# Optimization experiments

Measured on AMD Instinct MI355X. Metric: run time of the kernel, lower is better.

Reference implementation:

```python
import jax, jax.numpy as jnp
import numpy as np

NF = 3
THRESH = 0.05
MODES1 = [0, 64, 32]
MODES2 = [0, 64, 32]
LEVEL = 3
WIDTHS = [32, 64, 64]


def _cgelu(z):
    # split-complex GELU: gelu on real and imag parts independently
    return jax.nn.gelu(z.real) + 1j * jax.nn.gelu(z.imag)


def _forward(x_real, x_imag, Re,
             p_w1_r, p_w1_i, p_b1_r, p_b1_i, p_w2_r, p_w2_i, p_b2_r, p_b2_i,
             w0_r, w0_i, wd1_r, wd1_i, wu1_r, wu1_i, wd2_r, wd2_i, wu2_r, wu2_i,
             S1, S2):
    c = lambda r, i: (r + 1j * i).astype(jnp.complex64)
    x = c(x_real, x_imag)                       # (B, C0, S1, M2) half-spectrum
    B = x.shape[0]
    M1, M2 = S1 // 2, S2 // 2 + 1
    m1_list = [M1, MODES1[1], MODES1[2]]
    m2_list = [M2, MODES2[1], MODES2[2]]

    # --- get_k: fractional powers of signed wavenumbers ---
    h1, h2 = S1 // 2, S2 // 2
    kx1 = jnp.concatenate([jnp.arange(0, S1 - h1), jnp.arange(-h1, 0)]).reshape(S1, 1)
    kx2 = jnp.concatenate([jnp.arange(0, S2 - h2), jnp.arange(-h2, 0)]).reshape(1, S2)
    k = jnp.stack([jnp.broadcast_to(kx1, (S1, S2)),
                   jnp.broadcast_to(kx2, (S1, S2))], 0)[..., :M2]   # (2, S1, M2)
    pw = (jnp.arange(1, NF + 1, dtype=jnp.float32) / NF).reshape(NF, 1, 1, 1)
    k_mat = jnp.power(k[None].astype(jnp.complex64), pw)            # (NF, 2, S1, M2)
    k_mat = jnp.broadcast_to(k_mat.reshape(1, 2 * NF, S1, M2), (B, 2 * NF, S1, M2))

    # --- embed_re: fractional powers of Reynolds number ---
    re_pw = (jnp.arange(1, NF + 1, dtype=jnp.float32) / NF).reshape(1, NF, 1, 1)
    re_mat = jnp.power(Re, re_pw).astype(jnp.complex64)             # (B, NF, 1, 1)
    re_mat = jnp.broadcast_to(re_mat, (B, NF, S1, M2))

    feat = jnp.concatenate([k_mat, re_mat], axis=1)                 # (B, 3*NF, S1, M2)

    # --- complex 1x1-conv MLP p ---
    h = jnp.einsum('bixy,oi->boxy', feat, c(p_w1_r, p_w1_i)) + c(p_b1_r, p_b1_i)[None, :, None, None]
    h = _cgelu(h)
    re_feature = jnp.einsum('bixy,oi->boxy', h, c(p_w2_r, p_w2_i)) + c(p_b2_r, p_b2_i)[None, :, None, None]

    x = x * re_feature
    x = jnp.where(jnp.abs(x) > THRESH, x, jnp.zeros((), x.dtype))   # sparsity mask

    # level 0 (skip_in is all-ones complex)
    x1 = x + 1.0
    x1 = _cgelu(jnp.einsum('bixy,io->boxy', x1, c(w0_r, w0_i)))

    Wd = [None, c(wd1_r, wd1_i), c(wd2_r, wd2_i)]
    Wu = [None, c(wu1_r, wu1_i), c(wu2_r, wu2_i)]

    xs = [x1]
    for i in range(1, LEVEL):  # down path: corner mode truncation + channel mix
        m1, m2 = m1_list[i], m2_list[i]
        x2 = jnp.concatenate([x1[:, :, :m1, :m2], x1[:, :, -m1:, :m2]], axis=2)
        x1 = _cgelu(jnp.einsum('bixy,io->boxy', x2, Wd[i])) + 1.0
        xs.append(x1)

    skip_out = list(xs)
    for i in range(LEVEL - 1, 0, -1):  # up path: channel mix + corner add
        u = _cgelu(jnp.einsum('bixy,io->boxy', xs[i], Wu[i]))
        m1, m2 = m1_list[i], m2_list[i]
        prev = xs[i - 1]
        prev = prev.at[:, :, :m1, :m2].add(u[:, :, :m1, :m2])
        prev = prev.at[:, :, -m1:, :m2].add(u[:, :, -m1:, :m2])
        xs[i - 1] = prev
        skip_out[i - 1] = prev  # torch mutates in place, so skip_out aliases

    return (xs[0], skip_out[0], skip_out[1], skip_out[2])


def setup_inputs() -> dict:
    key = jax.random.key(0)
    B, S1, S2 = 8, 256, 256
    M2 = S2 // 2 + 1
    ks = jax.random.split(key, 24)
    f = lambda k, s: jax.random.normal(k, s, jnp.float32)
    w = lambda k, s: 0.05 * jax.random.normal(k, s, jnp.float32)
    return {
        'x_real': f(ks[0], (B, 32, S1, M2)),
        'x_imag': f(ks[1], (B, 32, S1, M2)),
        'Re': jax.random.uniform(ks[2], (B, 1, 1, 1), jnp.float32, 0.5, 2.0),
        'p_w1_r': w(ks[3], (32, 9)), 'p_w1_i': w(ks[4], (32, 9)),
        'p_b1_r': w(ks[5], (32,)), 'p_b1_i': w(ks[6], (32,)),
        'p_w2_r': w(ks[7], (32, 32)), 'p_w2_i': w(ks[8], (32, 32)),
        'p_b2_r': w(ks[9], (32,)), 'p_b2_i': w(ks[10], (32,)),
        'w0_r': w(ks[11], (32, 32)), 'w0_i': w(ks[12], (32, 32)),
        'wd1_r': w(ks[13], (32, 64)), 'wd1_i': w(ks[14], (32, 64)),
        'wu1_r': w(ks[15], (64, 32)), 'wu1_i': w(ks[16], (64, 32)),
        'wd2_r': w(ks[17], (64, 64)), 'wd2_i': w(ks[18], (64, 64)),
        'wu2_r': w(ks[19], (64, 64)), 'wu2_i': w(ks[20], (64, 64)),
        'S1': S1, 'S2': S2,
    }


def reference(x_real, x_imag, Re,
              p_w1_r, p_w1_i, p_b1_r, p_b1_i, p_w2_r, p_w2_i, p_b2_r, p_b2_i,
              w0_r, w0_i, wd1_r, wd1_i, wu1_r, wu1_i, wd2_r, wd2_i, wu2_r, wu2_i,
              S1, S2):
    return _forward(x_real, x_imag, Re,
                    p_w1_r, p_w1_i, p_b1_r, p_b1_i, p_w2_r, p_w2_i, p_b2_r, p_b2_i,
                    w0_r, w0_i, wd1_r, wd1_i, wu1_r, wu1_i, wd2_r, wd2_i, wu2_r, wu2_i,
                    S1, S2)
```

## Files before the change

### kernel.cpp

```cpp
#include <hip/hip_runtime.h>

typedef long long i64;

#define BB   8
#define SS1  256
#define MM2  129
#define SP0  (SS1*MM2)

#define O0 0LL
#define O1 8454144LL
#define O2 16908288LL
#define O3 21102592LL

__device__ __forceinline__ float ldf(const float* p, i64 i, i64 cap) {
    return (i >= 0 && i < cap) ? p[i] : 0.0f;
}
__device__ __forceinline__ void stf(float* p, i64 i, i64 cap, float v) {
    if (i >= 0 && i < cap) p[i] = v;
}

__device__ __forceinline__ float tanh_fast(float x) {
    float a = fabsf(x);
    float t = __expf(-2.0f * a);
    float r = (1.0f - t) * __builtin_amdgcn_rcpf(1.0f + t);
    return copysignf(r, x);
}
__device__ __forceinline__ float gelu_f(float x) {
    float inner = 0.7978845608028654f * (x + 0.044715f * x * x * x);
    return 0.5f * x * (1.0f + tanh_fast(inner));
}

__device__ __forceinline__ void compute_features(
    int b, int x, int y, const float* __restrict__ Re,
    float* fr, float* fi, float* rp)
{
    float kv0 = (x < 128) ? (float)x : (float)(x - 256);
    float kv1 = (y < 128) ? (float)y : -128.0f;
    const float P[3] = {1.0f/3.0f, 2.0f/3.0f, 1.0f};
    #pragma unroll
    for (int d = 0; d < 2; d++) {
        float k = d ? kv1 : kv0;
        float lg = __logf(fabsf(k));
        #pragma unroll
        for (int f = 0; f < 3; f++) {
            int c = f * 2 + d;
            float m = __expf(P[f] * lg);
            if (k == 0.0f)      { fr[c] = 0.0f; fi[c] = 0.0f; }
            else if (k > 0.0f)  { fr[c] = m;    fi[c] = 0.0f; }
            else {
                float ang = P[f] * 3.14159274101257f;
                fr[c] = m * __cosf(ang);
                fi[c] = m * __sinf(ang);
            }
        }
    }
    float lre = __logf(Re[b]);
    #pragma unroll
    for (int f = 0; f < 3; f++) rp[f] = __expf(P[f] * lre);
}

__global__ __launch_bounds__(256) void k_level0(
    const float* __restrict__ xr, const float* __restrict__ xi,
    const float* __restrict__ Re,
    const float* __restrict__ w1r, const float* __restrict__ w1i,
    const float* __restrict__ b1r, const float* __restrict__ b1i,
    const float* __restrict__ w2r, const float* __restrict__ w2i,
    const float* __restrict__ b2r, const float* __restrict__ b2i,
    const float* __restrict__ w0r, const float* __restrict__ w0i,
    float* __restrict__ of, i64 capf)
{
    int idx = blockIdx.x * 256 + threadIdx.x;
    if (idx >= BB * SP0) return;
    int y  = idx % MM2;
    int t2 = idx / MM2;
    int x  = t2 % SS1;
    int b  = t2 / SS1;

    float fr[6], fi[6], rp[3];
    compute_features(b, x, y, Re, fr, fi, rp);

    float hr[32], hi[32];
    #pragma unroll
    for (int o = 0; o < 32; o++) {
        float ar = b1r[o], ai = b1i[o];
        #pragma unroll
        for (int i = 0; i < 6; i++) {
            float wr = w1r[o * 9 + i], wi = w1i[o * 9 + i];
            ar += wr * fr[i] - wi * fi[i];
            ai += wr * fi[i] + wi * fr[i];
        }
        #pragma unroll
        for (int f = 0; f < 3; f++) {
            ar += w1r[o * 9 + 6 + f] * rp[f];
            ai += w1i[o * 9 + 6 + f] * rp[f];
        }
        hr[o] = gelu_f(ar);
        hi[o] = gelu_f(ai);
    }

    float acc[32];
    #pragma unroll
    for (int o = 0; o < 32; o++) acc[o] = 0.0f;

    const float TH2 = 0.05f * 0.05f;
    i64 base0 = (i64)b * 32 * SP0 + (i64)x * MM2 + y;
    for (int c = 0; c < 32; c++) {
        float rr0 = b2r[c], ri0 = b2i[c], rr1 = 0.0f, ri1 = 0.0f;
        #pragma unroll
        for (int i = 0; i < 16; i++) {
            float wr = w2r[c * 32 + i], wi = w2i[c * 32 + i];
            rr0 += wr * hr[i] - wi * hi[i];
            ri0 += wr * hi[i] + wi * hr[i];
        }
        #pragma unroll
        for (int i = 16; i < 32; i++) {
            float wr = w2r[c * 32 + i], wi = w2i[c * 32 + i];
            rr1 += wr * hr[i] - wi * hi[i];
            ri1 += wr * hi[i] + wi * hr[i];
        }
        float rrs = rr0 + rr1, ris = ri0 + ri1;
        float xre = xr[base0 + (i64)c * SP0];
        float xim = xi[base0 + (i64)c * SP0];
        float pr = xre * rrs - xim * ris;
        float pi = xre * ris + xim * rrs;
        if (pr * pr + pi * pi <= TH2) { pr = 0.0f; pi = 0.0f; }
        float vr_c = pr + 1.0f;
        float vi_c = pi;
        #pragma unroll
        for (int o = 0; o < 32; o++) {
            float wr = w0r[c * 32 + o], wi = w0i[c * 32 + o];
            acc[o] += wr * vr_c - wi * vi_c;
        }
    }

    #pragma unroll
    for (int o = 0; o < 32; o++) {
        float g = gelu_f(acc[o]);
        i64 oi = base0 + (i64)o * SP0;
        stf(of, O0 + oi, capf, g);
        stf(of, O1 + oi, capf, g);
    }
}

#define PH  0
#define PV  32
#define PX1 64
#define PV1 96
#define PV2 160

__global__ __launch_bounds__(512, 4) void k_branch1(
    const float* __restrict__ xr, const float* __restrict__ xi,
    const float* __restrict__ Re,
    const float* __restrict__ w1r, const float* __restrict__ w1i,
    const float* __restrict__ b1r, const float* __restrict__ b1i,
    const float* __restrict__ w2r, const float* __restrict__ w2i,
    const float* __restrict__ b2r, const float* __restrict__ b2i,
    const float* __restrict__ w0r, const float* __restrict__ w0i,
    const float* __restrict__ wd1r, const float* __restrict__ wd1i,
    const float* __restrict__ wu1r, const float* __restrict__ wu1i,
    float* __restrict__ of, i64 capf)
{
    int base = blockIdx.x * 8;
    int y0 = base & 63;
    int r1 = (base >> 6) & 127;
    int b  = base >> 13;
    if ((y0 < 32) && (r1 < 32 || r1 >= 96)) return;
    int x0 = (r1 < 64) ? r1 : r1 + 128;

    __shared__ float2 s_w2t[1024];
    __shared__ float2 s_w0[1024];
    __shared__ float2 s_wd1[2048];
    __shared__ float2 s_wu1[2048];
    __shared__ float2 s_pt[8][160];
    __shared__ float  s_u[8][32];

    for (int t = threadIdx.x; t < 1024; t += 512) {
        int c = t >> 5, i = t & 31;
        s_w2t[i * 32 + c] = make_float2(w2r[t], w2i[t]);
        s_w0[t] = make_float2(w0r[t], w0i[t]);
    }
    for (int t = threadIdx.x; t < 2048; t += 512) {
        s_wd1[t] = make_float2(wd1r[t], wd1i[t]);
        s_wu1[t] = make_float2(wu1r[t], wu1i[t]);
    }

    int p = threadIdx.x >> 6;
    int lane = threadIdx.x & 63;
    int y = y0 + p;

    if (lane < 32) {
        float fr[6], fi[6], rp[3];
        compute_features(b, x0, y, Re, fr, fi, rp);
        int o = lane;
        float ar = b1r[o], ai = b1i[o];
        #pragma unroll
        for (int i = 0; i < 6; i++) {
            float wr = w1r[o * 9 + i], wi = w1i[o * 9 + i];
            ar += wr * fr[i] - wi * fi[i];
            ai += wr * fi[i] + wi * fr[i];
        }
        #pragma unroll
        for (int f = 0; f < 3; f++) {
            ar += w1r[o * 9 + 6 + f] * rp[f];
            ai += w1i[o * 9 + 6 + f] * rp[f];
        }
        s_pt[p][PH + o] = make_float2(gelu_f(ar), gelu_f(ai));
    }
    __syncthreads();

    if (lane < 32) {
        int c = lane;
        float rr = b2r[c], ri = b2i[c];
        #pragma unroll
        for (int i = 0; i < 32; i++) {
            float2 w = s_w2t[i * 32 + c];
            float2 h = s_pt[p][PH + i];
            rr += w.x * h.x - w.y * h.y;
            ri += w.x * h.y + w.y * h.x;
        }
        i64 xoff = ((i64)b * 32 + c) * SP0 + (i64)x0 * MM2 + y;
        float xre = xr[xoff], xim = xi[xoff];
        float pr = xre * rr - xim * ri;
        float pi = xre * ri + xim * rr;
        const float TH2 = 0.05f * 0.05f;
        if (pr * pr + pi * pi <= TH2) { pr = 0.0f; pi = 0.0f; }
        s_pt[p][PV + c] = make_float2(pr + 1.0f, pi);
    }
    __syncthreads();

    {
        int o = lane & 31, part = lane >> 5;
        const float* vv = (const float*)&s_pt[p][PV];
        int ia = part ? 1 : 0, ib = part ? 0 : 1;
        float sgn = part ? 1.0f : -1.0f;
        float a = 0.0f;
        #pragma unroll
        for (int c2 = 0; c2 < 32; c2++) {
            float2 w = s_w0[c2 * 32 + o];
            a += w.x * vv[2 * c2 + ia] + sgn * w.y * vv[2 * c2 + ib];
        }
        a = gelu_f(a);
        ((float*)&s_pt[p][PX1 + o])[part] = a;
    }
    __syncthreads();

    {
        float ar = 0.0f, ai = 0.0f;
        #pragma unroll
        for (int i2 = 0; i2 < 32; i2++) {
            float2 w = s_wd1[i2 * 64 + lane];
            float2 x1 = s_pt[p][PX1 + i2];
            ar += w.x * x1.x - w.y * x1.y;
            ai += w.x * x1.y + w.y * x1.x;
        }
        s_pt[p][PV1 + lane] = make_float2(gelu_f(ar) + 1.0f, gelu_f(ai));
    }
    __syncthreads();

    {
        int o = threadIdx.x >> 3, ty = threadIdx.x & 7;
        float v = s_pt[ty][PV1 + o].x;
        stf(of, O2 + ((i64)((i64)b * 64 + o) * 128 + r1) * 64 + (y0 + ty), capf, v);
    }

    {
        int o = lane & 31, half = lane >> 5;
        float acc = 0.0f;
        #pragma unroll
        for (int c2 = 0; c2 < 32; c2++) {
            int c = half * 32 + c2;
            float2 w = s_wu1[c * 32 + o];
            float2 v1 = s_pt[p][PV1 + c];
            acc += w.x * v1.x - w.y * v1.y;
        }
        acc += __shfl_xor(acc, 32);
        if (lane < 32) s_u[p][o] = gelu_f(acc);
    }
    __syncthreads();

    if (threadIdx.x < 256) {
        int o = threadIdx.x >> 3, ty = threadIdx.x & 7;
        i64 oi = ((i64)b * 32 + o) * SP0 + (i64)x0 * MM2 + (y0 + ty);
        float cur = ldf(of, O0 + oi, capf) + s_u[ty][o];
        stf(of, O0 + oi, capf, cur);
        stf(of, O1 + oi, capf, cur);
    }
}

__global__ __launch_bounds__(512, 4) void k_branch2(
    const float* __restrict__ xr, const float* __restrict__ xi,
    const float* __restrict__ Re,
    const float* __restrict__ w1r, const float* __restrict__ w1i,
    const float* __restrict__ b1r, const float* __restrict__ b1i,
    const float* __restrict__ w2r, const float* __restrict__ w2i,
    const float* __restrict__ b2r, const float* __restrict__ b2i,
    const float* __restrict__ w0r, const float* __restrict__ w0i,
    const float* __restrict__ wd1r, const float* __restrict__ wd1i,
    const float* __restrict__ wu1r, const float* __restrict__ wu1i,
    const float* __restrict__ wd2r, const float* __restrict__ wd2i,
    const float* __restrict__ wu2r, const float* __restrict__ wu2i,
    float* __restrict__ of, i64 capf)
{
    int base = blockIdx.x * 8;
    int y0 = base & 31;
    int r2 = (base >> 5) & 63;
    int b  = base >> 11;
    int r1 = (r2 < 32) ? r2 : r2 + 64;
    int x0 = (r1 < 64) ? r1 : r1 + 128;

    __shared__ float2 s_w2t[1024];
    __shared__ float2 s_w0[1024];
    __shared__ float2 s_wd1[2048];
    __shared__ float2 s_wu1[2048];
    __shared__ float2 s_pt[8][224];
    __shared__ float  s_u[8][32];

    for (int t = threadIdx.x; t < 1024; t += 512) {
        int c = t >> 5, i = t & 31;
        s_w2t[i * 32 + c] = make_float2(w2r[t], w2i[t]);
        s_w0[t] = make_float2(w0r[t], w0i[t]);
    }
    for (int t = threadIdx.x; t < 2048; t += 512) {
        s_wd1[t] = make_float2(wd1r[t], wd1i[t]);
        s_wu1[t] = make_float2(wu1r[t], wu1i[t]);
    }

    int p = threadIdx.x >> 6;
    int lane = threadIdx.x & 63;
    int y = y0 + p;

    if (lane < 32) {
        float fr[6], fi[6], rp[3];
        compute_features(b, x0, y, Re, fr, fi, rp);
        int o = lane;
        float ar = b1r[o], ai = b1i[o];
        #pragma unroll
        for (int i = 0; i < 6; i++) {
            float wr = w1r[o * 9 + i], wi = w1i[o * 9 + i];
            ar += wr * fr[i] - wi * fi[i];
            ai += wr * fi[i] + wi * fr[i];
        }
        #pragma unroll
        for (int f = 0; f < 3; f++) {
            ar += w1r[o * 9 + 6 + f] * rp[f];
            ai += w1i[o * 9 + 6 + f] * rp[f];
        }
        s_pt[p][PH + o] = make_float2(gelu_f(ar), gelu_f(ai));
    }
    __syncthreads();

    if (lane < 32) {
        int c = lane;
        float rr = b2r[c], ri = b2i[c];
        #pragma unroll
        for (int i = 0; i < 32; i++) {
            float2 w = s_w2t[i * 32 + c];
            float2 h = s_pt[p][PH + i];
            rr += w.x * h.x - w.y * h.y;
            ri += w.x * h.y + w.y * h.x;
        }
        i64 xoff = ((i64)b * 32 + c) * SP0 + (i64)x0 * MM2 + y;
        float xre = xr[xoff], xim = xi[xoff];
        float pr = xre * rr - xim * ri;
        float pi = xre * ri + xim * rr;
        const float TH2 = 0.05f * 0.05f;
        if (pr * pr + pi * pi <= TH2) { pr = 0.0f; pi = 0.0f; }
        s_pt[p][PV + c] = make_float2(pr + 1.0f, pi);
    }
    __syncthreads();

    {
        int o = lane & 31, part = lane >> 5;
        const float* vv = (const float*)&s_pt[p][PV];
        int ia = part ? 1 : 0, ib = part ? 0 : 1;
        float sgn = part ? 1.0f : -1.0f;
        float a = 0.0f;
        #pragma unroll
        for (int c2 = 0; c2 < 32; c2++) {
            float2 w = s_w0[c2 * 32 + o];
            a += w.x * vv[2 * c2 + ia] + sgn * w.y * vv[2 * c2 + ib];
        }
        a = gelu_f(a);
        ((float*)&s_pt[p][PX1 + o])[part] = a;
    }
    __syncthreads();

    {
        float ar = 0.0f, ai = 0.0f;
        #pragma unroll
        for (int i2 = 0; i2 < 32; i2++) {
            float2 w = s_wd1[i2 * 64 + lane];
            float2 x1 = s_pt[p][PX1 + i2];
            ar += w.x * x1.x - w.y * x1.y;
            ai += w.x * x1.y + w.y * x1.x;
        }
        s_pt[p][PV1 + lane] = make_float2(gelu_f(ar) + 1.0f, gelu_f(ai));
    }
    __syncthreads();

    {
        float ar = 0.0f, ai = 0.0f;
        #pragma unroll 8
        for (int c2 = 0; c2 < 64; c2++) {
            float wr = wd2r[c2 * 64 + lane], wi = wd2i[c2 * 64 + lane];
            float2 v1 = s_pt[p][PV1 + c2];
            ar += wr * v1.x - wi * v1.y;
            ai += wr * v1.y + wi * v1.x;
        }
        s_pt[p][PV2 + lane] = make_float2(gelu_f(ar) + 1.0f, gelu_f(ai));
    }
    __syncthreads();

    {
        int o = threadIdx.x >> 3, ty = threadIdx.x & 7;
        float v = s_pt[ty][PV2 + o].x;
        stf(of, O3 + ((i64)((i64)b * 64 + o) * 64 + r2) * 32 + (y0 + ty), capf, v);
    }

    {
        float ar = 0.0f, ai = 0.0f;
        #pragma unroll 8
        for (int c2 = 0; c2 < 64; c2++) {
            float wr = wu2r[c2 * 64 + lane], wi = wu2i[c2 * 64 + lane];
            float2 v2 = s_pt[p][PV2 + c2];
            ar += wr * v2.x - wi * v2.y;
            ai += wr * v2.y + wi * v2.x;
        }
        float2 v1 = s_pt[p][PV1 + lane];
        v1.x += gelu_f(ar);
        v1.y += gelu_f(ai);
        s_pt[p][PV1 + lane] = v1;
    }
    __syncthreads();

    {
        int o = threadIdx.x >> 3, ty = threadIdx.x & 7;
        float v = s_pt[ty][PV1 + o].x;
        stf(of, O2 + ((i64)((i64)b * 64 + o) * 128 + r1) * 64 + (y0 + ty), capf, v);
    }

    {
        int o = lane & 31, half = lane >> 5;
        float acc = 0.0f;
        #pragma unroll
        for (int c2 = 0; c2 < 32; c2++) {
            int c = half * 32 + c2;
            float2 w = s_wu1[c * 32 + o];
            float2 v1 = s_pt[p][PV1 + c];
            acc += w.x * v1.x - w.y * v1.y;
        }
        acc += __shfl_xor(acc, 32);
        if (lane < 32) s_u[p][o] = gelu_f(acc);
    }
    __syncthreads();

    if (threadIdx.x < 256) {
        int o = threadIdx.x >> 3, ty = threadIdx.x & 7;
        i64 oi = ((i64)b * 32 + o) * SP0 + (i64)x0 * MM2 + (y0 + ty);
        float cur = ldf(of, O0 + oi, capf) + s_u[ty][o];
        stf(of, O0 + oi, capf, cur);
        stf(of, O1 + oi, capf, cur);
    }
}

extern "C" void kernel_launch(void* const* d_in, const int* in_sizes, int n_in,
                              void* d_out, int out_size, void* d_ws, size_t ws_size,
                              hipStream_t stream) {
    const float* xr   = (const float*)d_in[0];
    const float* xi   = (const float*)d_in[1];
    const float* Re   = (const float*)d_in[2];
    const float* w1r  = (const float*)d_in[3];
    const float* w1i  = (const float*)d_in[4];
    const float* b1r  = (const float*)d_in[5];
    const float* b1i  = (const float*)d_in[6];
    const float* w2r  = (const float*)d_in[7];
    const float* w2i  = (const float*)d_in[8];
    const float* b2r  = (const float*)d_in[9];
    const float* b2i  = (const float*)d_in[10];
    const float* w0r  = (const float*)d_in[11];
    const float* w0i  = (const float*)d_in[12];
    const float* wd1r = (const float*)d_in[13];
    const float* wd1i = (const float*)d_in[14];
    const float* wu1r = (const float*)d_in[15];
    const float* wu1i = (const float*)d_in[16];
    const float* wd2r = (const float*)d_in[17];
    const float* wd2i = (const float*)d_in[18];
    const float* wu2r = (const float*)d_in[19];
    const float* wu2i = (const float*)d_in[20];

    float* of  = (float*)d_out;
    i64 capf   = (i64)out_size;

    k_level0<<<dim3((BB * SP0 + 255) / 256), 256, 0, stream>>>(
        xr, xi, Re, w1r, w1i, b1r, b1i, w2r, w2i, b2r, b2i, w0r, w0i, of, capf);
    k_branch1<<<dim3(8192), 512, 0, stream>>>(
        xr, xi, Re, w1r, w1i, b1r, b1i, w2r, w2i, b2r, b2i, w0r, w0i,
        wd1r, wd1i, wu1r, wu1i, of, capf);
    k_branch2<<<dim3(2048), 512, 0, stream>>>(
        xr, xi, Re, w1r, w1i, b1r, b1i, w2r, w2i, b2r, b2i, w0r, w0i,
        wd1r, wd1i, wu1r, wu1i, wd2r, wd2i, wu2r, wu2i, of, capf);
}
```

Before: 529.9 us.

## Process two batches per thread in level0 and drop intra-wave barriers

k_level0 now handles batch pairs (b, b+4) in each thread. The Fourier-wavenumber features and their first MLP partial sums are computed once and reused, and every weight load serves both batches; the grid is halved to match. Separately, several __syncthreads calls in the branch kernels are removed, relying on each point's 64 lanes forming one wavefront. The trade-off is much higher register pressure in level0 (two sets of hidden and accumulator arrays), which may cause spills or lower occupancy. Dropping the barriers also depends on wave64 lockstep execution for correct shared-memory ordering.

Result: slower. 564.0 us (+6.4%).

```diff
diff --git a/kernel.cpp b/kernel.cpp
--- a/kernel.cpp
+++ b/kernel.cpp
@@ -59,7 +59,7 @@
     for (int f = 0; f < 3; f++) rp[f] = __expf(P[f] * lre);
 }
 
-__global__ __launch_bounds__(256) void k_level0(
+__global__ __launch_bounds__(256, 2) void k_level0(
     const float* __restrict__ xr, const float* __restrict__ xi,
     const float* __restrict__ Re,
     const float* __restrict__ w1r, const float* __restrict__ w1i,
@@ -70,75 +70,115 @@
     float* __restrict__ of, i64 capf)
 {
     int idx = blockIdx.x * 256 + threadIdx.x;
-    if (idx >= BB * SP0) return;
+    if (idx >= 4 * SP0) return;
     int y  = idx % MM2;
     int t2 = idx / MM2;
     int x  = t2 % SS1;
-    int b  = t2 / SS1;
-
-    float fr[6], fi[6], rp[3];
-    compute_features(b, x, y, Re, fr, fi, rp);
-
-    float hr[32], hi[32];
+    int bp = t2 / SS1;
+
+    float fr[6], fi[6];
+    {
+        float kv0 = (x < 128) ? (float)x : (float)(x - 256);
+        float kv1 = (y < 128) ? (float)y : -128.0f;
+        const float P[3] = {1.0f/3.0f, 2.0f/3.0f, 1.0f};
+        #pragma unroll
+        for (int d = 0; d < 2; d++) {
+            float k = d ? kv1 : kv0;
+            float lg = __logf(fabsf(k));
+            #pragma unroll
+            for (int f = 0; f < 3; f++) {
+                int c = f * 2 + d;
+                float m = __expf(P[f] * lg);
+                if (k == 0.0f)      { fr[c] = 0.0f; fi[c] = 0.0f; }
+                else if (k > 0.0f)  { fr[c] = m;    fi[c] = 0.0f; }
+                else {
+                    float ang = P[f] * 3.14159274101257f;
+                    fr[c] = m * __cosf(ang);
+                    fi[c] = m * __sinf(ang);
+                }
+            }
+        }
+    }
+    const float P3[3] = {1.0f/3.0f, 2.0f/3.0f, 1.0f};
+    float lre0 = __logf(Re[bp]);
+    float lre1 = __logf(Re[bp + 4]);
+    float rp0[3], rp1[3];
+    #pragma unroll
+    for (int f = 0; f < 3; f++) {
+        rp0[f] = __expf(P3[f] * lre0);
+        rp1[f] = __expf(P3[f] * lre1);
+    }
+
+    float h0r[32], h0i[32], h1r[32], h1i[32];
     #pragma unroll
     for (int o = 0; o < 32; o++) {
-        float ar = b1r[o], ai = b1i[o];
+        float cr = b1r[o], ci = b1i[o];
         #pragma unroll
         for (int i = 0; i < 6; i++) {
             float wr = w1r[o * 9 + i], wi = w1i[o * 9 + i];
-            ar += wr * fr[i] - wi * fi[i];
-            ai += wr * fi[i] + wi * fr[i];
-        }
+            cr += wr * fr[i] - wi * fi[i];
+            ci += wr * fi[i] + wi * fr[i];
+        }
+        float a0r = cr, a0i = ci, a1r = cr, a1i = ci;
         #pragma unroll
         for (int f = 0; f < 3; f++) {
-            ar += w1r[o * 9 + 6 + f] * rp[f];
-            ai += w1i[o * 9 + 6 + f] * rp[f];
-        }
-        hr[o] = gelu_f(ar);
-        hi[o] = gelu_f(ai);
-    }
-
-    float acc[32];
+            float wr = w1r[o * 9 + 6 + f], wi = w1i[o * 9 + 6 + f];
+            a0r += wr * rp0[f];  a0i += wi * rp0[f];
+            a1r += wr * rp1[f];  a1i += wi * rp1[f];
+        }
+        h0r[o] = gelu_f(a0r);  h0i[o] = gelu_f(a0i);
+        h1r[o] = gelu_f(a1r);  h1i[o] = gelu_f(a1i);
+    }
+
+    float acc0[32], acc1[32];
     #pragma unroll
-    for (int o = 0; o < 32; o++) acc[o] = 0.0f;
+    for (int o = 0; o < 32; o++) { acc0[o] = 0.0f; acc1[o] = 0.0f; }
 
     const float TH2 = 0.05f * 0.05f;
-    i64 base0 = (i64)b * 32 * SP0 + (i64)x * MM2 + y;
+    i64 sp    = (i64)x * MM2 + y;
+    i64 baseA = (i64)bp * 32 * SP0 + sp;
+    i64 baseB = (i64)(bp + 4) * 32 * SP0 + sp;
     for (int c = 0; c < 32; c++) {
-        float rr0 = b2r[c], ri0 = b2i[c], rr1 = 0.0f, ri1 = 0.0f;
-        #pragma unroll
-        for (int i = 0; i < 16; i++) {
+        float rrA = b2r[c], riA = b2i[c];
+        float rrB = rrA,    riB = riA;
+        #pragma unroll
+        for (int i = 0; i < 32; i++) {
             float wr = w2r[c * 32 + i], wi = w2i[c * 32 + i];
-            rr0 += wr * hr[i] - wi * hi[i];
-            ri0 += wr * hi[i] + wi * hr[i];
-        }
-        #pragma unroll
-        for (int i = 16; i < 32; i++) {
-            float wr = w2r[c * 32 + i], wi = w2i[c * 32 + i];
-            rr1 += wr * hr[i] - wi * hi[i];
-            ri1 += wr * hi[i] + wi * hr[i];
-        }
-        float rrs = rr0 + rr1, ris = ri0 + ri1;
-        float xre = xr[base0 + (i64)c * SP0];
-        float xim = xi[base0 + (i64)c * SP0];
-        float pr = xre * rrs - xim * ris;
-        float pi = xre * ris + xim * rrs;
-        if (pr * pr + pi * pi <= TH2) { pr = 0.0f; pi = 0.0f; }
-        float vr_c = pr + 1.0f;
-        float vi_c = pi;
+            rrA += wr * h0r[i] - wi * h0i[i];
+            riA += wr * h0i[i] + wi * h0r[i];
+            rrB += wr * h1r[i] - wi * h1i[i];
+            riB += wr * h1i[i] + wi * h1r[i];
+        }
+        float xreA = xr[baseA + (i64)c * SP0];
+        float ximA = xi[baseA + (i64)c * SP0];
+        float xreB = xr[baseB + (i64)c * SP0];
+        float ximB = xi[baseB + (i64)c * SP0];
+        float prA = xreA * rrA - ximA * riA;
+        float piA = xreA * riA + ximA * rrA;
+        float prB = xreB * rrB - ximB * riB;
+        float piB = xreB * riB + ximB * rrB;
+        if (prA * prA + piA * piA <= TH2) { prA = 0.0f; piA = 0.0f; }
+        if (prB * prB + piB * piB <= TH2) { prB = 0.0f; piB = 0.0f; }
+        float vrA = prA + 1.0f, viA = piA;
+        float vrB = prB + 1.0f, viB = piB;
         #pragma unroll
         for (int o = 0; o < 32; o++) {
             float wr = w0r[c * 32 + o], wi = w0i[c * 32 + o];
-            acc[o] += wr * vr_c - wi * vi_c;
+            acc0[o] += wr * vrA - wi * viA;
+            acc1[o] += wr * vrB - wi * viB;
         }
     }
 
     #pragma unroll
     for (int o = 0; o < 32; o++) {
-        float g = gelu_f(acc[o]);
-        i64 oi = base0 + (i64)o * SP0;
-        stf(of, O0 + oi, capf, g);
-        stf(of, O1 + oi, capf, g);
+        float g0 = gelu_f(acc0[o]);
+        float g1 = gelu_f(acc1[o]);
+        i64 oiA = baseA + (i64)o * SP0;
+        i64 oiB = baseB + (i64)o * SP0;
+        stf(of, O0 + oiA, capf, g0);
+        stf(of, O1 + oiA, capf, g0);
+        stf(of, O0 + oiB, capf, g1);
+        stf(of, O1 + oiB, capf, g1);
     }
 }
 
@@ -226,7 +266,6 @@
         if (pr * pr + pi * pi <= TH2) { pr = 0.0f; pi = 0.0f; }
         s_pt[p][PV + c] = make_float2(pr + 1.0f, pi);
     }
-    __syncthreads();
 
     {
         int o = lane & 31, part = lane >> 5;
@@ -242,7 +281,6 @@
         a = gelu_f(a);
         ((float*)&s_pt[p][PX1 + o])[part] = a;
     }
-    __syncthreads();
 
     {
         float ar = 0.0f, ai = 0.0f;
@@ -367,7 +405,6 @@
         if (pr * pr + pi * pi <= TH2) { pr = 0.0f; pi = 0.0f; }
         s_pt[p][PV + c] = make_float2(pr + 1.0f, pi);
     }
-    __syncthreads();
 
     {
         int o = lane & 31, part = lane >> 5;
@@ -383,7 +420,6 @@
         a = gelu_f(a);
         ((float*)&s_pt[p][PX1 + o])[part] = a;
     }
-    __syncthreads();
 
     {
         float ar = 0.0f, ai = 0.0f;
@@ -396,7 +432,6 @@
         }
         s_pt[p][PV1 + lane] = make_float2(gelu_f(ar) + 1.0f, gelu_f(ai));
     }
-    __syncthreads();
 
     {
         float ar = 0.0f, ai = 0.0f;
@@ -491,7 +526,7 @@
     float* of  = (float*)d_out;
     i64 capf   = (i64)out_size;
 
-    k_level0<<<dim3((BB * SP0 + 255) / 256), 256, 0, stream>>>(
+    k_level0<<<dim3((4 * SP0 + 255) / 256), 256, 0, stream>>>(
         xr, xi, Re, w1r, w1i, b1r, b1i, w2r, w2i, b2r, b2i, w0r, w0i, of, capf);
     k_branch1<<<dim3(8192), 512, 0, stream>>>(
         xr, xi, Re, w1r, w1i, b1r, b1i, w2r, w2i, b2r, b2i, w0r, w0i,
```

## Partition level-0 points by branch ownership and loop branch blocks over multiple rows

Applied to the files above, without the earlier changes.

The level-0 kernel now runs only on spectral points that no branch kernel covers. The branch kernels compute the full level-0 result themselves and write it directly, instead of reading back and adding to the level-0 output. Each branch block processes four 8-column groups in a loop, which amortises shared-memory weight staging over more points and drops several intermediate barriers. The level-0 kernel also stages half of w2 in shared memory as float4 pairs. The risks are heavier per-block work with fewer blocks, and correctness depends on the point partition exactly matching the branch coverage.

Measured after the change: 570.8 us. 1.08x slower.

```diff
diff --git a/kernel.cpp b/kernel.cpp
--- a/kernel.cpp
+++ b/kernel.cpp
@@ -6,6 +6,7 @@
 #define SS1  256
 #define MM2  129
 #define SP0  (SS1*MM2)
+#define NPTS_B 24832
 
 #define O0 0LL
 #define O1 8454144LL
@@ -69,12 +70,26 @@
     const float* __restrict__ w0r, const float* __restrict__ w0i,
     float* __restrict__ of, i64 capf)
 {
+    __shared__ float4 s_w2[512];
+    for (int t = threadIdx.x; t < 512; t += 256) {
+        int e = t * 2;
+        s_w2[t] = make_float4(w2r[e], w2i[e], w2r[e + 1], w2i[e + 1]);
+    }
+    __syncthreads();
+
     int idx = blockIdx.x * 256 + threadIdx.x;
-    if (idx >= BB * SP0) return;
-    int y  = idx % MM2;
-    int t2 = idx / MM2;
-    int x  = t2 % SS1;
-    int b  = t2 / SS1;
+    if (idx >= BB * NPTS_B) return;
+    int b = idx / NPTS_B;
+    int j = idx - b * NPTS_B;
+    int x, y;
+    if (j < 16640) {
+        x = j / 65;
+        y = 64 + (j - x * 65);
+    } else {
+        int j2 = j - 16640;
+        x = 64 + (j2 >> 6);
+        y = j2 & 63;
+    }
 
     float fr[6], fi[6], rp[3];
     compute_features(b, x, y, Re, fr, fi, rp);
@@ -107,16 +122,21 @@
     for (int c = 0; c < 32; c++) {
         float rr0 = b2r[c], ri0 = b2i[c], rr1 = 0.0f, ri1 = 0.0f;
         #pragma unroll
-        for (int i = 0; i < 16; i++) {
-            float wr = w2r[c * 32 + i], wi = w2i[c * 32 + i];
-            rr0 += wr * hr[i] - wi * hi[i];
-            ri0 += wr * hi[i] + wi * hr[i];
+        for (int i = 0; i < 16; i += 2) {
+            float4 w = s_w2[c * 16 + (i >> 1)];
+            rr0 += w.x * hr[i]     - w.y * hi[i];
+            ri0 += w.x * hi[i]     + w.y * hr[i];
+            rr1 += w.z * hr[i + 1] - w.w * hi[i + 1];
+            ri1 += w.z * hi[i + 1] + w.w * hr[i + 1];
         }
         #pragma unroll
-        for (int i = 16; i < 32; i++) {
-            float wr = w2r[c * 32 + i], wi = w2i[c * 32 + i];
-            rr1 += wr * hr[i] - wi * hi[i];
-            ri1 += wr * hi[i] + wi * hr[i];
+        for (int i = 16; i < 32; i += 2) {
+            float wr0 = w2r[c * 32 + i],     wi0 = w2i[c * 32 + i];
+            float wr1 = w2r[c * 32 + i + 1], wi1 = w2i[c * 32 + i + 1];
+            rr0 += wr0 * hr[i]     - wi0 * hi[i];
+            ri0 += wr0 * hi[i]     + wi0 * hr[i];
+            rr1 += wr1 * hr[i + 1] - wi1 * hi[i + 1];
+            ri1 += wr1 * hi[i + 1] + wi1 * hr[i + 1];
         }
         float rrs = rr0 + rr1, ris = ri0 + ri1;
         float xre = xr[base0 + (i64)c * SP0];
@@ -160,11 +180,10 @@
     const float* __restrict__ wu1r, const float* __restrict__ wu1i,
     float* __restrict__ of, i64 capf)
 {
-    int base = blockIdx.x * 8;
-    int y0 = base & 63;
-    int r1 = (base >> 6) & 127;
-    int b  = base >> 13;
-    if ((y0 < 32) && (r1 < 32 || r1 >= 96)) return;
+    int h  = blockIdx.x & 1;
+    int r1 = (blockIdx.x >> 1) & 127;
+    int b  = blockIdx.x >> 8;
+    if (h == 0 && (r1 < 32 || r1 >= 96)) return;
     int x0 = (r1 < 64) ? r1 : r1 + 128;
 
     __shared__ float2 s_w2t[1024];
@@ -186,104 +205,107 @@
 
     int p = threadIdx.x >> 6;
     int lane = threadIdx.x & 63;
-    int y = y0 + p;
-
-    if (lane < 32) {
-        float fr[6], fi[6], rp[3];
-        compute_features(b, x0, y, Re, fr, fi, rp);
-        int o = lane;
-        float ar = b1r[o], ai = b1i[o];
-        #pragma unroll
-        for (int i = 0; i < 6; i++) {
-            float wr = w1r[o * 9 + i], wi = w1i[o * 9 + i];
-            ar += wr * fr[i] - wi * fi[i];
-            ai += wr * fi[i] + wi * fr[i];
-        }
-        #pragma unroll
-        for (int f = 0; f < 3; f++) {
-            ar += w1r[o * 9 + 6 + f] * rp[f];
-            ai += w1i[o * 9 + 6 + f] * rp[f];
-        }
-        s_pt[p][PH + o] = make_float2(gelu_f(ar), gelu_f(ai));
-    }
     __syncthreads();
 
-    if (lane < 32) {
-        int c = lane;
-        float rr = b2r[c], ri = b2i[c];
-        #pragma unroll
-        for (int i = 0; i < 32; i++) {
-            float2 w = s_w2t[i * 32 + c];
-            float2 h = s_pt[p][PH + i];
-            rr += w.x * h.x - w.y * h.y;
-            ri += w.x * h.y + w.y * h.x;
-        }
-        i64 xoff = ((i64)b * 32 + c) * SP0 + (i64)x0 * MM2 + y;
-        float xre = xr[xoff], xim = xi[xoff];
-        float pr = xre * rr - xim * ri;
-        float pi = xre * ri + xim * rr;
-        const float TH2 = 0.05f * 0.05f;
-        if (pr * pr + pi * pi <= TH2) { pr = 0.0f; pi = 0.0f; }
-        s_pt[p][PV + c] = make_float2(pr + 1.0f, pi);
-    }
-    __syncthreads();
-
-    {
-        int o = lane & 31, part = lane >> 5;
-        const float* vv = (const float*)&s_pt[p][PV];
-        int ia = part ? 1 : 0, ib = part ? 0 : 1;
-        float sgn = part ? 1.0f : -1.0f;
-        float a = 0.0f;
-        #pragma unroll
-        for (int c2 = 0; c2 < 32; c2++) {
-            float2 w = s_w0[c2 * 32 + o];
-            a += w.x * vv[2 * c2 + ia] + sgn * w.y * vv[2 * c2 + ib];
-        }
-        a = gelu_f(a);
-        ((float*)&s_pt[p][PX1 + o])[part] = a;
-    }
-    __syncthreads();
-
-    {
-        float ar = 0.0f, ai = 0.0f;
-        #pragma unroll
-        for (int i2 = 0; i2 < 32; i2++) {
-            float2 w = s_wd1[i2 * 64 + lane];
-            float2 x1 = s_pt[p][PX1 + i2];
-            ar += w.x * x1.x - w.y * x1.y;
-            ai += w.x * x1.y + w.y * x1.x;
-        }
-        s_pt[p][PV1 + lane] = make_float2(gelu_f(ar) + 1.0f, gelu_f(ai));
-    }
-    __syncthreads();
-
-    {
-        int o = threadIdx.x >> 3, ty = threadIdx.x & 7;
-        float v = s_pt[ty][PV1 + o].x;
-        stf(of, O2 + ((i64)((i64)b * 64 + o) * 128 + r1) * 64 + (y0 + ty), capf, v);
-    }
-
-    {
-        int o = lane & 31, half = lane >> 5;
-        float acc = 0.0f;
-        #pragma unroll
-        for (int c2 = 0; c2 < 32; c2++) {
-            int c = half * 32 + c2;
-            float2 w = s_wu1[c * 32 + o];
-            float2 v1 = s_pt[p][PV1 + c];
-            acc += w.x * v1.x - w.y * v1.y;
-        }
-        acc += __shfl_xor(acc, 32);
-        if (lane < 32) s_u[p][o] = gelu_f(acc);
-    }
-    __syncthreads();
-
-    if (threadIdx.x < 256) {
-        int o = threadIdx.x >> 3, ty = threadIdx.x & 7;
-        i64 oi = ((i64)b * 32 + o) * SP0 + (i64)x0 * MM2 + (y0 + ty);
-        float cur = ldf(of, O0 + oi, capf) + s_u[ty][o];
-        stf(of, O0 + oi, capf, cur);
-        stf(of, O1 + oi, capf, cur);
+    for (int rep = 0; rep < 4; rep++) {
+        int ybase = h * 32 + rep * 8;
+        int y = ybase + p;
+
+        if (lane < 32) {
+            float fr[6], fi[6], rp[3];
+            compute_features(b, x0, y, Re, fr, fi, rp);
+            int o = lane;
+            float ar = b1r[o], ai = b1i[o];
+            #pragma unroll
+            for (int i = 0; i < 6; i++) {
+                float wr = w1r[o * 9 + i], wi = w1i[o * 9 + i];
+                ar += wr * fr[i] - wi * fi[i];
+                ai += wr * fi[i] + wi * fr[i];
+            }
+            #pragma unroll
+            for (int f = 0; f < 3; f++) {
+                ar += w1r[o * 9 + 6 + f] * rp[f];
+                ai += w1i[o * 9 + 6 + f] * rp[f];
+            }
+            s_pt[p][PH + o] = make_float2(gelu_f(ar), gelu_f(ai));
+        }
+
+        if (lane < 32) {
+            int c = lane;
+            float rr = b2r[c], ri = b2i[c];
+            #pragma unroll
+            for (int i = 0; i < 32; i++) {
+                float2 w = s_w2t[i * 32 + c];
+                float2 hh = s_pt[p][PH + i];
+                rr += w.x * hh.x - w.y * hh.y;
+                ri += w.x * hh.y + w.y * hh.x;
+            }
+            i64 xoff = ((i64)b * 32 + c) * SP0 + (i64)x0 * MM2 + y;
+            float xre = xr[xoff], xim = xi[xoff];
+            float pr = xre * rr - xim * ri;
+            float pi = xre * ri + xim * rr;
+            const float TH2 = 0.05f * 0.05f;
+            if (pr * pr + pi * pi <= TH2) { pr = 0.0f; pi = 0.0f; }
+            s_pt[p][PV + c] = make_float2(pr + 1.0f, pi);
+        }
+
+        {
+            int o = lane & 31, part = lane >> 5;
+            const float* vv = (const float*)&s_pt[p][PV];
+            int ia = part ? 1 : 0, ib = part ? 0 : 1;
+            float sgn = part ? 1.0f : -1.0f;
+            float a = 0.0f;
+            #pragma unroll
+            for (int c2 = 0; c2 < 32; c2++) {
+                float2 w = s_w0[c2 * 32 + o];
+                a += w.x * vv[2 * c2 + ia] + sgn * w.y * vv[2 * c2 + ib];
+            }
+            a = gelu_f(a);
+            ((float*)&s_pt[p][PX1 + o])[part] = a;
+        }
+
+        {
+            float ar = 0.0f, ai = 0.0f;
+            #pragma unroll
+            for (int i2 = 0; i2 < 32; i2++) {
+                float2 w = s_wd1[i2 * 64 + lane];
+                float2 x1 = s_pt[p][PX1 + i2];
+                ar += w.x * x1.x - w.y * x1.y;
+                ai += w.x * x1.y + w.y * x1.x;
+            }
+            s_pt[p][PV1 + lane] = make_float2(gelu_f(ar) + 1.0f, gelu_f(ai));
+        }
+        __syncthreads();
+
+        {
+            int o = threadIdx.x >> 3, ty = threadIdx.x & 7;
+            float v = s_pt[ty][PV1 + o].x;
+            stf(of, O2 + ((i64)((i64)b * 64 + o) * 128 + r1) * 64 + (ybase + ty), capf, v);
+        }
+
+        {
+            int o = lane & 31, half = lane >> 5;
+            float acc = 0.0f;
+            #pragma unroll
+            for (int c2 = 0; c2 < 32; c2++) {
+                int c = half * 32 + c2;
+                float2 w = s_wu1[c * 32 + o];
+                float2 v1 = s_pt[p][PV1 + c];
+                acc += w.x * v1.x - w.y * v1.y;
+            }
+            acc += __shfl_xor(acc, 32);
+            if (lane < 32) s_u[p][o] = gelu_f(acc);
+        }
+        __syncthreads();
+
+        if (threadIdx.x < 256) {
+            int o = threadIdx.x >> 3, ty = threadIdx.x & 7;
+            i64 oi = ((i64)b * 32 + o) * SP0 + (i64)x0 * MM2 + (ybase + ty);
+            float cur = s_pt[ty][PX1 + o].x + s_u[ty][o];
+            stf(of, O0 + oi, capf, cur);
+            stf(of, O1 + oi, capf, cur);
+        }
+        __syncthreads();
     }
 }
 
@@ -301,10 +323,8 @@
     const float* __restrict__ wu2r, const float* __restrict__ wu2i,
     float* __restrict__ of, i64 capf)
 {
-    int base = blockIdx.x * 8;
-    int y0 = base & 31;
-    int r2 = (base >> 5) & 63;
-    int b  = base >> 11;
+    int r2 = blockIdx.x & 63;
+    int b  = blockIdx.x >> 6;
     int r1 = (r2 < 32) ? r2 : r2 + 64;
     int x0 = (r1 < 64) ? r1 : r1 + 128;
 
@@ -327,139 +347,141 @@
 
     int p = threadIdx.x >> 6;
     int lane = threadIdx.x & 63;
-    int y = y0 + p;
-
-    if (lane < 32) {
-        float fr[6], fi[6], rp[3];
-        compute_features(b, x0, y, Re, fr, fi, rp);
-        int o = lane;
-        float ar = b1r[o], ai = b1i[o];
-        #pragma unroll
-        for (int i = 0; i < 6; i++) {
-            float wr = w1r[o * 9 + i], wi = w1i[o * 9 + i];
-            ar += wr * fr[i] - wi * fi[i];
-            ai += wr * fi[i] + wi * fr[i];
-        }
-        #pragma unroll
-        for (int f = 0; f < 3; f++) {
-            ar += w1r[o * 9 + 6 + f] * rp[f];
-            ai += w1i[o * 9 + 6 + f] * rp[f];
-        }
-        s_pt[p][PH + o] = make_float2(gelu_f(ar), gelu_f(ai));
-    }
     __syncthreads();
 
-    if (lane < 32) {
-        int c = lane;
-        float rr = b2r[c], ri = b2i[c];
-        #pragma unroll
-        for (int i = 0; i < 32; i++) {
-            float2 w = s_w2t[i * 32 + c];
-            float2 h = s_pt[p][PH + i];
-            rr += w.x * h.x - w.y * h.y;
-            ri += w.x * h.y + w.y * h.x;
-        }
-        i64 xoff = ((i64)b * 32 + c) * SP0 + (i64)x0 * MM2 + y;
-        float xre = xr[xoff], xim = xi[xoff];
-        float pr = xre * rr - xim * ri;
-        float pi = xre * ri + xim * rr;
-        const float TH2 = 0.05f * 0.05f;
-        if (pr * pr + pi * pi <= TH2) { pr = 0.0f; pi = 0.0f; }
-        s_pt[p][PV + c] = make_float2(pr + 1.0f, pi);
-    }
-    __syncthreads();
-
-    {
-        int o = lane & 31, part = lane >> 5;
-        const float* vv = (const float*)&s_pt[p][PV];
-        int ia = part ? 1 : 0, ib = part ? 0 : 1;
-        float sgn = part ? 1.0f : -1.0f;
-        float a = 0.0f;
-        #pragma unroll
-        for (int c2 = 0; c2 < 32; c2++) {
-            float2 w = s_w0[c2 * 32 + o];
-            a += w.x * vv[2 * c2 + ia] + sgn * w.y * vv[2 * c2 + ib];
-        }
-        a = gelu_f(a);
-        ((float*)&s_pt[p][PX1 + o])[part] = a;
-    }
-    __syncthreads();
-
-    {
-        float ar = 0.0f, ai = 0.0f;
-        #pragma unroll
-        for (int i2 = 0; i2 < 32; i2++) {
-            float2 w = s_wd1[i2 * 64 + lane];
-            float2 x1 = s_pt[p][PX1 + i2];
-            ar += w.x * x1.x - w.y * x1.y;
-            ai += w.x * x1.y + w.y * x1.x;
-        }
-        s_pt[p][PV1 + lane] = make_float2(gelu_f(ar) + 1.0f, gelu_f(ai));
-    }
-    __syncthreads();
-
-    {
-        float ar = 0.0f, ai = 0.0f;
-        #pragma unroll 8
-        for (int c2 = 0; c2 < 64; c2++) {
-            float wr = wd2r[c2 * 64 + lane], wi = wd2i[c2 * 64 + lane];
-            float2 v1 = s_pt[p][PV1 + c2];
-            ar += wr * v1.x - wi * v1.y;
-            ai += wr * v1.y + wi * v1.x;
-        }
-        s_pt[p][PV2 + lane] = make_float2(gelu_f(ar) + 1.0f, gelu_f(ai));
-    }
-    __syncthreads();
-
-    {
-        int o = threadIdx.x >> 3, ty = threadIdx.x & 7;
-        float v = s_pt[ty][PV2 + o].x;
-        stf(of, O3 + ((i64)((i64)b * 64 + o) * 64 + r2) * 32 + (y0 + ty), capf, v);
-    }
-
-    {
-        float ar = 0.0f, ai = 0.0f;
-        #pragma unroll 8
-        for (int c2 = 0; c2 < 64; c2++) {
-            float wr = wu2r[c2 * 64 + lane], wi = wu2i[c2 * 64 + lane];
-            float2 v2 = s_pt[p][PV2 + c2];
-            ar += wr * v2.x - wi * v2.y;
-            ai += wr * v2.y + wi * v2.x;
-        }
-        float2 v1 = s_pt[p][PV1 + lane];
-        v1.x += gelu_f(ar);
-        v1.y += gelu_f(ai);
-        s_pt[p][PV1 + lane] = v1;
-    }
-    __syncthreads();
-
-    {
-        int o = threadIdx.x >> 3, ty = threadIdx.x & 7;
-        float v = s_pt[ty][PV1 + o].x;
-        stf(of, O2 + ((i64)((i64)b * 64 + o) * 128 + r1) * 64 + (y0 + ty), capf, v);
-    }
-
-    {
-        int o = lane & 31, half = lane >> 5;
-        float acc = 0.0f;
-        #pragma unroll
-        for (int c2 = 0; c2 < 32; c2++) {
-            int c = half * 32 + c2;
-            float2 w = s_wu1[c * 32 + o];
-            float2 v1 = s_pt[p][PV1 + c];
-            acc += w.x * v1.x - w.y * v1.y;
-        }
-        acc += __shfl_xor(acc, 32);
-        if (lane < 32) s_u[p][o] = gelu_f(acc);
-    }
-    __syncthreads();
-
-    if (threadIdx.x < 256) {
-        int o = threadIdx.x >> 3, ty = threadIdx.x & 7;
-        i64 oi = ((i64)b * 32 + o) * SP0 + (i64)x0 * MM2 + (y0 + ty);
-        float cur = ldf(of, O0 + oi, capf) + s_u[ty][o];
-        stf(of, O0 + oi, capf, cur);
-        stf(of, O1 + oi, capf, cur);
+    for (int rep = 0; rep < 4; rep++) {
+        int ybase = rep * 8;
+        int y = ybase + p;
+
+        if (lane < 32) {
+            float fr[6], fi[6], rp[3];
+            compute_features(b, x0, y, Re, fr, fi, rp);
+            int o = lane;
+            float ar = b1r[o], ai = b1i[o];
+            #pragma unroll
+            for (int i = 0; i < 6; i++) {
+                float wr = w1r[o * 9 + i], wi = w1i[o * 9 + i];
+                ar += wr * fr[i] - wi * fi[i];
+                ai += wr * fi[i] + wi * fr[i];
+            }
+            #pragma unroll
+            for (int f = 0; f < 3; f++) {
+                ar += w1r[o * 9 + 6 + f] * rp[f];
+                ai += w1i[o * 9 + 6 + f] * rp[f];
+            }
+            s_pt[p][PH + o] = make_float2(gelu_f(ar), gelu_f(ai));
+        }
+
+        if (lane < 32) {
+            int c = lane;
+            float rr = b2r[c], ri = b2i[c];
+            #pragma unroll
+            for (int i = 0; i < 32; i++) {
+                float2 w = s_w2t[i * 32 + c];
+                float2 hh = s_pt[p][PH + i];
+                rr += w.x * hh.x - w.y * hh.y;
+                ri += w.x * hh.y + w.y * hh.x;
+            }
+            i64 xoff = ((i64)b * 32 + c) * SP0 + (i64)x0 * MM2 + y;
+            float xre = xr[xoff], xim = xi[xoff];
+            float pr = xre * rr - xim * ri;
+            float pi = xre * ri + xim * rr;
+            const float TH2 = 0.05f * 0.05f;
+            if (pr * pr + pi * pi <= TH2) { pr = 0.0f; pi = 0.0f; }
+            s_pt[p][PV + c] = make_float2(pr + 1.0f, pi);
+        }
+
+        {
+            int o = lane & 31, part = lane >> 5;
+            const float* vv = (const float*)&s_pt[p][PV];
+            int ia = part ? 1 : 0, ib = part ? 0 : 1;
+            float sgn = part ? 1.0f : -1.0f;
+            float a = 0.0f;
+            #pragma unroll
+            for (int c2 = 0; c2 < 32; c2++) {
+                float2 w = s_w0[c2 * 32 + o];
+                a += w.x * vv[2 * c2 + ia] + sgn * w.y * vv[2 * c2 + ib];
+            }
+            a = gelu_f(a);
+            ((float*)&s_pt[p][PX1 + o])[part] = a;
+        }
+
+        {
+            float ar = 0.0f, ai = 0.0f;
+            #pragma unroll
+            for (int i2 = 0; i2 < 32; i2++) {
+                float2 w = s_wd1[i2 * 64 + lane];
+                float2 x1 = s_pt[p][PX1 + i2];
+                ar += w.x * x1.x - w.y * x1.y;
+                ai += w.x * x1.y + w.y * x1.x;
+            }
+            s_pt[p][PV1 + lane] = make_float2(gelu_f(ar) + 1.0f, gelu_f(ai));
+        }
+
+        {
+            float ar = 0.0f, ai = 0.0f;
+            #pragma unroll 8
+            for (int c2 = 0; c2 < 64; c2++) {
+                float wr = wd2r[c2 * 64 + lane], wi = wd2i[c2 * 64 + lane];
+                float2 v1 = s_pt[p][PV1 + c2];
+                ar += wr * v1.x - wi * v1.y;
+                ai += wr * v1.y + wi * v1.x;
+            }
+            s_pt[p][PV2 + lane] = make_float2(gelu_f(ar) + 1.0f, gelu_f(ai));
+        }
+        __syncthreads();
+
+        {
+            int o = threadIdx.x >> 3, ty = threadIdx.x & 7;
+            float v = s_pt[ty][PV2 + o].x;
+            stf(of, O3 + ((i64)((i64)b * 64 + o) * 64 + r2) * 32 + (ybase + ty), capf, v);
+        }
+
+        {
+            float ar = 0.0f, ai = 0.0f;
+            #pragma unroll 8
+            for (int c2 = 0; c2 < 64; c2++) {
+                float wr = wu2r[c2 * 64 + lane], wi = wu2i[c2 * 64 + lane];
+                float2 v2 = s_pt[p][PV2 + c2];
+                ar += wr * v2.x - wi * v2.y;
+                ai += wr * v2.y + wi * v2.x;
+            }
+            float2 v1 = s_pt[p][PV1 + lane];
+            v1.x += gelu_f(ar);
+            v1.y += gelu_f(ai);
+            s_pt[p][PV1 + lane] = v1;
+        }
+        __syncthreads();
+
+        {
+            int o = threadIdx.x >> 3, ty = threadIdx.x & 7;
+            float v = s_pt[ty][PV1 + o].x;
+            stf(of, O2 + ((i64)((i64)b * 64 + o) * 128 + r1) * 64 + (ybase + ty), capf, v);
+        }
+
+        {
+            int o = lane & 31, half = lane >> 5;
+            float acc = 0.0f;
+            #pragma unroll
+            for (int c2 = 0; c2 < 32; c2++) {
+                int c = half * 32 + c2;
+                float2 w = s_wu1[c * 32 + o];
+                float2 v1 = s_pt[p][PV1 + c];
+                acc += w.x * v1.x - w.y * v1.y;
+            }
+            acc += __shfl_xor(acc, 32);
+            if (lane < 32) s_u[p][o] = gelu_f(acc);
+        }
+        __syncthreads();
+
+        if (threadIdx.x < 256) {
+            int o = threadIdx.x >> 3, ty = threadIdx.x & 7;
+            i64 oi = ((i64)b * 32 + o) * SP0 + (i64)x0 * MM2 + (ybase + ty);
+            float cur = s_pt[ty][PX1 + o].x + s_u[ty][o];
+            stf(of, O0 + oi, capf, cur);
+            stf(of, O1 + oi, capf, cur);
+        }
+        __syncthreads();
     }
 }
 
@@ -491,12 +513,12 @@
     float* of  = (float*)d_out;
     i64 capf   = (i64)out_size;
 
-    k_level0<<<dim3((BB * SP0 + 255) / 256), 256, 0, stream>>>(
+    k_level0<<<dim3((BB * NPTS_B + 255) / 256), 256, 0, stream>>>(
         xr, xi, Re, w1r, w1i, b1r, b1i, w2r, w2i, b2r, b2i, w0r, w0i, of, capf);
-    k_branch1<<<dim3(8192), 512, 0, stream>>>(
+    k_branch1<<<dim3(2048), 512, 0, stream>>>(
         xr, xi, Re, w1r, w1i, b1r, b1i, w2r, w2i, b2r, b2i, w0r, w0i,
         wd1r, wd1i, wu1r, wu1i, of, capf);
-    k_branch2<<<dim3(2048), 512, 0, stream>>>(
+    k_branch2<<<dim3(512), 512, 0, stream>>>(
         xr, xi, Re, w1r, w1i, b1r, b1i, w2r, w2i, b2r, b2i, w0r, w0i,
         wd1r, wd1i, wu1r, wu1i, wd2r, wd2i, wu2r, wu2i, of, capf);
 }
```

## Skip level-0 points covered by branch kernels and split channels across thread pairs

Applied to the files above, without the earlier changes.

k_level0 now only processes spectral points outside the low-mode corners. The branch kernels already compute the level-0 activation for those corners, so they take it from shared memory instead of re-reading what level0 wrote to global memory. Each point's 32 output channels are split across two adjacent threads that combine partial sums with a shuffle, and the weights are staged in LDS as packed float4/float2. The aim is to cut redundant level-0 compute and a global read-after-write. This relies on the hardcoded region split and on the branch kernels holding an exact copy of x1.

After: 688.5 us. +29.9%, slower.

```diff
diff --git a/kernel.cpp b/kernel.cpp
--- a/kernel.cpp
+++ b/kernel.cpp
@@ -6,6 +6,7 @@
 #define SS1  256
 #define MM2  129
 #define SP0  (SS1*MM2)
+#define NPTS_B 24832
 
 #define O0 0LL
 #define O1 8454144LL
@@ -59,7 +60,7 @@
     for (int f = 0; f < 3; f++) rp[f] = __expf(P[f] * lre);
 }
 
-__global__ __launch_bounds__(256) void k_level0(
+__global__ __launch_bounds__(256, 5) void k_level0(
     const float* __restrict__ xr, const float* __restrict__ xi,
     const float* __restrict__ Re,
     const float* __restrict__ w1r, const float* __restrict__ w1i,
@@ -69,74 +70,96 @@
     const float* __restrict__ w0r, const float* __restrict__ w0i,
     float* __restrict__ of, i64 capf)
 {
-    int idx = blockIdx.x * 256 + threadIdx.x;
-    if (idx >= BB * SP0) return;
-    int y  = idx % MM2;
-    int t2 = idx / MM2;
-    int x  = t2 % SS1;
-    int b  = t2 / SS1;
+    __shared__ float4 s_w2[512];
+    __shared__ float4 s_w0[512];
+    __shared__ float2 s_w1[288];
+    __shared__ float2 s_b1[32];
+    for (int t = threadIdx.x; t < 512; t += 256) {
+        int e = t * 2;
+        s_w2[t] = make_float4(w2r[e], w2i[e], w2r[e + 1], w2i[e + 1]);
+        s_w0[t] = make_float4(w0r[e], w0i[e], w0r[e + 1], w0i[e + 1]);
+        if (t < 288) s_w1[t] = make_float2(w1r[t], w1i[t]);
+        if (t < 32)  s_b1[t] = make_float2(b1r[t], b1i[t]);
+    }
+    __syncthreads();
+
+    int tid = blockIdx.x * 256 + threadIdx.x;
+    int half = tid & 1;
+    int pid  = tid >> 1;
+    int b = pid / NPTS_B;
+    int j = pid - b * NPTS_B;
+    int x, y;
+    if (j < 16640) {
+        x = j / 65;
+        y = 64 + (j - x * 65);
+    } else {
+        int j2 = j - 16640;
+        x = 64 + (j2 >> 6);
+        y = j2 & 63;
+    }
 
     float fr[6], fi[6], rp[3];
     compute_features(b, x, y, Re, fr, fi, rp);
 
-    float hr[32], hi[32];
+    float hr[16], hi[16];
     #pragma unroll
-    for (int o = 0; o < 32; o++) {
-        float ar = b1r[o], ai = b1i[o];
-        #pragma unroll
-        for (int i = 0; i < 6; i++) {
-            float wr = w1r[o * 9 + i], wi = w1i[o * 9 + i];
-            ar += wr * fr[i] - wi * fi[i];
-            ai += wr * fi[i] + wi * fr[i];
+    for (int t = 0; t < 16; t++) {
+        int i = half * 16 + t;
+        float2 bb = s_b1[i];
+        float ar = bb.x, ai = bb.y;
+        #pragma unroll
+        for (int k = 0; k < 6; k++) {
+            float2 w = s_w1[i * 9 + k];
+            ar += w.x * fr[k] - w.y * fi[k];
+            ai += w.x * fi[k] + w.y * fr[k];
         }
         #pragma unroll
         for (int f = 0; f < 3; f++) {
-            ar += w1r[o * 9 + 6 + f] * rp[f];
-            ai += w1i[o * 9 + 6 + f] * rp[f];
-        }
-        hr[o] = gelu_f(ar);
-        hi[o] = gelu_f(ai);
-    }
-
-    float acc[32];
+            float2 w = s_w1[i * 9 + 6 + f];
+            ar += w.x * rp[f];
+            ai += w.y * rp[f];
+        }
+        hr[t] = gelu_f(ar);
+        hi[t] = gelu_f(ai);
+    }
+
+    float acc[16];
     #pragma unroll
-    for (int o = 0; o < 32; o++) acc[o] = 0.0f;
+    for (int t = 0; t < 16; t++) acc[t] = 0.0f;
 
     const float TH2 = 0.05f * 0.05f;
     i64 base0 = (i64)b * 32 * SP0 + (i64)x * MM2 + y;
     for (int c = 0; c < 32; c++) {
-        float rr0 = b2r[c], ri0 = b2i[c], rr1 = 0.0f, ri1 = 0.0f;
-        #pragma unroll
-        for (int i = 0; i < 16; i++) {
-            float wr = w2r[c * 32 + i], wi = w2i[c * 32 + i];
-            rr0 += wr * hr[i] - wi * hi[i];
-            ri0 += wr * hi[i] + wi * hr[i];
-        }
-        #pragma unroll
-        for (int i = 16; i < 32; i++) {
-            float wr = w2r[c * 32 + i], wi = w2i[c * 32 + i];
-            rr1 += wr * hr[i] - wi * hi[i];
-            ri1 += wr * hi[i] + wi * hr[i];
-        }
-        float rrs = rr0 + rr1, ris = ri0 + ri1;
+        float prr = 0.0f, pri = 0.0f;
+        #pragma unroll
+        for (int t = 0; t < 16; t += 2) {
+            float4 w = s_w2[c * 16 + half * 8 + (t >> 1)];
+            prr += w.x * hr[t]     - w.y * hi[t];
+            pri += w.x * hi[t]     + w.y * hr[t];
+            prr += w.z * hr[t + 1] - w.w * hi[t + 1];
+            pri += w.z * hi[t + 1] + w.w * hr[t + 1];
+        }
+        float rr = prr + __shfl_xor(prr, 1) + b2r[c];
+        float ri = pri + __shfl_xor(pri, 1) + b2i[c];
         float xre = xr[base0 + (i64)c * SP0];
         float xim = xi[base0 + (i64)c * SP0];
-        float pr = xre * rrs - xim * ris;
-        float pi = xre * ris + xim * rrs;
+        float pr = xre * rr - xim * ri;
+        float pi = xre * ri + xim * rr;
         if (pr * pr + pi * pi <= TH2) { pr = 0.0f; pi = 0.0f; }
         float vr_c = pr + 1.0f;
         float vi_c = pi;
         #pragma unroll
-        for (int o = 0; o < 32; o++) {
-            float wr = w0r[c * 32 + o], wi = w0i[c * 32 + o];
-            acc[o] += wr * vr_c - wi * vi_c;
+        for (int t = 0; t < 16; t += 2) {
+            float4 w = s_w0[c * 16 + half * 8 + (t >> 1)];
+            acc[t]     += w.x * vr_c - w.y * vi_c;
+            acc[t + 1] += w.z * vr_c - w.w * vi_c;
         }
     }
 
     #pragma unroll
-    for (int o = 0; o < 32; o++) {
-        float g = gelu_f(acc[o]);
-        i64 oi = base0 + (i64)o * SP0;
+    for (int t = 0; t < 16; t++) {
+        float g = gelu_f(acc[t]);
+        i64 oi = base0 + (i64)(half * 16 + t) * SP0;
         stf(of, O0 + oi, capf, g);
         stf(of, O1 + oi, capf, g);
     }
@@ -281,7 +304,7 @@
     if (threadIdx.x < 256) {
         int o = threadIdx.x >> 3, ty = threadIdx.x & 7;
         i64 oi = ((i64)b * 32 + o) * SP0 + (i64)x0 * MM2 + (y0 + ty);
-        float cur = ldf(of, O0 + oi, capf) + s_u[ty][o];
+        float cur = s_pt[ty][PX1 + o].x + s_u[ty][o];
         stf(of, O0 + oi, capf, cur);
         stf(of, O1 + oi, capf, cur);
     }
@@ -457,7 +480,7 @@
     if (threadIdx.x < 256) {
         int o = threadIdx.x >> 3, ty = threadIdx.x & 7;
         i64 oi = ((i64)b * 32 + o) * SP0 + (i64)x0 * MM2 + (y0 + ty);
-        float cur = ldf(of, O0 + oi, capf) + s_u[ty][o];
+        float cur = s_pt[ty][PX1 + o].x + s_u[ty][o];
         stf(of, O0 + oi, capf, cur);
         stf(of, O1 + oi, capf, cur);
     }
@@ -491,7 +514,7 @@
     float* of  = (float*)d_out;
     i64 capf   = (i64)out_size;
 
-    k_level0<<<dim3((BB * SP0 + 255) / 256), 256, 0, stream>>>(
+    k_level0<<<dim3((2 * BB * NPTS_B) / 256), 256, 0, stream>>>(
         xr, xi, Re, w1r, w1i, b1r, b1i, w2r, w2i, b2r, b2i, w0r, w0i, of, capf);
     k_branch1<<<dim3(8192), 512, 0, stream>>>(
         xr, xi, Re, w1r, w1i, b1r, b1i, w2r, w2i, b2r, b2i, w0r, w0i,
```
